# Kernel optimization log

Measured on AMD Instinct MI355X. Metric: run time of the kernel, lower is better.

Reference implementation:

```python
import jax, jax.numpy as jnp
import numpy as np

K = 3      # kernel size (hardcoded 3x3 in the torch module via repeat(...,9,...))
PAD = 1
STRIDE = 1


def _unfold(x):
    # torch.nn.functional.unfold equivalent: (B,C,H,W) -> (B,C,K,K,oh,ow)
    B, C, H, W = x.shape
    p = jax.lax.conv_general_dilated_patches(
        x, (K, K), (STRIDE, STRIDE), ((PAD, PAD), (PAD, PAD)))
    oh, ow = p.shape[2], p.shape[3]
    return p.reshape(B, C, K, K, oh, ow)


def setup_inputs() -> dict:
    key = jax.random.key(0)
    k1, k2, k3, k4 = jax.random.split(key, 4)
    B, Cin, Cout, H, W = 4, 64, 64, 128, 128
    inputs = jax.random.normal(k1, (B, Cin, H, W), jnp.float32)
    depth = jax.random.uniform(k2, (B, 1, H, W), jnp.float32)  # positive depths
    weight = jax.random.uniform(k3, (K, Cout, Cin, K, K), jnp.float32, minval=-0.05, maxval=0.05)
    bias = jax.random.uniform(k4, (Cout,), jnp.float32, minval=-0.05, maxval=0.05)
    return {"inputs": inputs, "depth": depth, "weight": weight, "bias": bias, "f": 1}


def reference(inputs, depth, weight, bias, f):
    # --- DepthKernelFn: per-depth-plane binary masks ---
    depth_wins = _unfold(depth)          # (B,1,K,K,oh,ow)
    s_wins = depth_wins / f              # grid spacing s_i = d / f
    cy, cx = K // 2, K // 2
    d0 = depth_wins[:, :, cy, cx]        # center depth      (B,1,oh,ow)
    s0 = s_wins[:, :, cy, cx]            # center spacing    (B,1,oh,ow)
    offs = jnp.arange(K, dtype=inputs.dtype) - (K - 1) / 2.0  # l - (K-1)/2
    # z_l at center: d0 + (l-1)*s0  -> (K,B,1,oh,ow)
    z0 = d0[None] + offs[:, None, None, None, None] * s0[None]
    half = s0[None] / 2
    a = (z0 - half)[:, :, :, None, None]  # (K,B,1,1,1,oh,ow)
    b = (z0 + half)[:, :, :, None, None]
    dw = depth_wins[None]                 # (1,B,1,K,K,oh,ow)
    # mask_l = 1 where a <= depth < b else 0  (same as the where-cascade in torch)
    mask = ((dw >= a) & (dw < b)).astype(inputs.dtype)  # (K,B,1,K,K,oh,ow)

    # --- RepeatKernelConvFn: masked windowed conv via einsum ---
    inp_wins = _unfold(inputs)            # (B,C,K,K,oh,ow)
    x = inp_wins[None] * mask             # (K,B,C,K,K,oh,ow), depth C=1 broadcasts
    out = jnp.einsum('hijklmn,hojkl->iomn', x, weight)
    out = out + bias.reshape(1, -1, 1, 1)
    return out
```

## Files before the change

kernel.cpp:

```cpp
#include <hip/hip_runtime.h>
#include <math.h>

#define B_N  4
#define CIN  64
#define COUT 64
#define H_N  128
#define W_N  128

typedef _Float16 half8 __attribute__((ext_vector_type(8)));
typedef float    f32x4 __attribute__((ext_vector_type(4)));

#define KTOT   1728
#define NSTEP  54
#define WA_BYTES ((size_t)NSTEP * 4 * 64 * 8 * 2)

__global__ void wprep(const float* __restrict__ w, _Float16* __restrict__ wa) {
    int idx = blockIdx.x * 256 + threadIdx.x;
    if (idx >= NSTEP * 4 * 64) return;
    int lane = idx & 63;
    int mt   = (idx >> 6) & 3;
    int s    = idx >> 8;
    int m    = mt * 16 + (lane & 15);
    int kl0  = (lane >> 4) * 8;
    _Float16 v[8];
#pragma unroll
    for (int j = 0; j < 8; ++j) {
        int k = s * 32 + kl0 + j;
        int g = k >> 6;
        int c = k & 63;
        int t = g / 3;
        int h = g % 3;
        v[j] = (_Float16)w[(((size_t)(h * COUT) + m) * CIN + c) * 9 + t];
    }
    *(int4*)&wa[(size_t)idx * 8] = *(int4*)v;
}

#define XS_LINE 64
#define XS_ROW  (130 * XS_LINE)

__global__ __launch_bounds__(256, 2)
void conv_mfma(const float* __restrict__ inp, const float* __restrict__ depth,
               const _Float16* __restrict__ wa, const float* __restrict__ bias,
               const int* __restrict__ fptr, float* __restrict__ out) {
    __shared__ _Float16 Xs[3 * XS_ROW];

    int bid  = blockIdx.x;
    int y    = bid & (H_N - 1);
    int b    = bid >> 7;
    int tid  = threadIdx.x;
    int lane = tid & 63;
    int wid  = tid >> 6;
    int mh   = wid & 1;
    int nq   = wid >> 1;
    int p0   = nq * 64;
    int ln15 = lane & 15;
    int quad = lane >> 4;

    {
        int x     = tid & 127;
        int chalf = tid >> 7;
        int xi    = x + 1;
        int key   = xi & 7;
        float fbuf[3][32];
#pragma unroll
        for (int dyi = 0; dyi < 3; ++dyi) {
            int yy = y + dyi - 1;
            if (yy >= 0 && yy < H_N) {
                const float* src = inp + (((size_t)b * CIN + chalf * 32) * H_N + yy) * W_N + x;
#pragma unroll
                for (int cc = 0; cc < 32; ++cc)
                    fbuf[dyi][cc] = src[(size_t)cc * H_N * W_N];
            } else {
#pragma unroll
                for (int cc = 0; cc < 32; ++cc) fbuf[dyi][cc] = 0.f;
            }
        }
#pragma unroll
        for (int dyi = 0; dyi < 3; ++dyi) {
            _Float16 hb[32];
#pragma unroll
            for (int cc = 0; cc < 32; ++cc) hb[cc] = (_Float16)fbuf[dyi][cc];
            _Float16* dst = &Xs[dyi * XS_ROW + xi * XS_LINE];
#pragma unroll
            for (int k = 0; k < 4; ++k)
                *(int4*)&dst[((chalf * 4 + k) ^ key) * 8] = *(int4*)&hb[k * 8];
        }
        if (tid < 48) {
            int dyi = tid / 16;
            int rem = tid % 16;
            int xz  = (rem >= 8) ? 129 : 0;
            int k8  = rem & 7;
            int4 z  = {0, 0, 0, 0};
            *(int4*)&Xs[dyi * XS_ROW + xz * XS_LINE + k8 * 8] = z;
        }
    }

    const half8* wa8 = (const half8*)wa;
    half8 A[6][2];
    {
        const half8* bA = wa8 + ((size_t)0 * 24 + mh * 2) * 64 + lane;
#pragma unroll
        for (int j = 0; j < 6; ++j)
#pragma unroll
            for (int mtl = 0; mtl < 2; ++mtl)
                A[j][mtl] = bA[(j * 4 + mtl) * 64];
    }

    double fd = (double)(*fptr);
    unsigned hpk[4];
#pragma unroll
    for (int nt = 0; nt < 4; ++nt) {
        int x = p0 + nt * 16 + ln15;
        float d0f = depth[((size_t)b * H_N + y) * W_N + x];
        double dd  = (double)d0f;
        double inv = fd / dd;
        bool   pos = (inv > 0.0);
        unsigned pk = 0;
        for (int t = 0; t < 9; ++t) {
            int dy = t / 3 - 1, dx = t % 3 - 1;
            int yy = y + dy, xx = x + dx;
            float dwf = (yy >= 0 && yy < H_N && xx >= 0 && xx < W_N)
                        ? depth[((size_t)b * H_N + yy) * W_N + xx] : 0.f;
            int h = -1;
            if (pos) {
                double u  = ((double)dwf - dd) * inv + 1.5;
                double uf = floor(u);
                if (uf >= 0.0 && uf <= 2.0) h = (int)uf;
            }
            pk |= (unsigned)(h + 1) << (2 * t);
        }
        hpk[nt] = pk;
    }

    __syncthreads();

    f32x4 acc[2][4];
#pragma unroll
    for (int mtl = 0; mtl < 2; ++mtl)
#pragma unroll
        for (int nt = 0; nt < 4; ++nt) acc[mtl][nt] = (f32x4){0.f, 0.f, 0.f, 0.f};

    half8 bb[2][8];

#define READ_B(tt) {                                                              \
        int dyi_ = (tt) / 3; int dx_ = (tt) % 3 - 1;                              \
        _Pragma("unroll")                                                         \
        for (int nt_ = 0; nt_ < 4; ++nt_) {                                       \
            int xs_  = p0 + nt_ * 16 + ln15 + dx_ + 1;                            \
            int key_ = xs_ & 7;                                                   \
            int ba_  = dyi_ * XS_ROW + xs_ * XS_LINE;                             \
            bb[(tt) & 1][nt_ * 2 + 0] = *(const half8*)&Xs[ba_ + ((quad    ) ^ key_) * 8]; \
            bb[(tt) & 1][nt_ * 2 + 1] = *(const half8*)&Xs[ba_ + ((quad + 4) ^ key_) * 8]; \
        }                                                                         \
    }

    READ_B(0);

    half8 z8 = {(_Float16)0.f, (_Float16)0.f, (_Float16)0.f, (_Float16)0.f,
                (_Float16)0.f, (_Float16)0.f, (_Float16)0.f, (_Float16)0.f};

#pragma unroll
    for (int t = 0; t < 9; ++t) {
        int hb[4];
#pragma unroll
        for (int nt = 0; nt < 4; ++nt) hb[nt] = (hpk[nt] >> (2 * t)) & 3;

#pragma unroll
        for (int h = 0; h < 3; ++h) {
#pragma unroll
            for (int kk = 0; kk < 2; ++kk) {
                int j = h * 2 + kk;
#pragma unroll
                for (int nt = 0; nt < 4; ++nt) {
                    half8 c = (hb[nt] == h + 1) ? bb[t & 1][nt * 2 + kk] : z8;
                    acc[0][nt] = __builtin_amdgcn_mfma_f32_16x16x32_f16(A[j][0], c, acc[0][nt], 0, 0, 0);
                    acc[1][nt] = __builtin_amdgcn_mfma_f32_16x16x32_f16(A[j][1], c, acc[1][nt], 0, 0, 0);
                }
            }
        }

        if (t < 8) {
            const half8* bA = wa8 + ((size_t)(t + 1) * 24 + mh * 2) * 64 + lane;
#pragma unroll
            for (int j = 0; j < 6; ++j)
#pragma unroll
                for (int mtl = 0; mtl < 2; ++mtl)
                    A[j][mtl] = bA[(j * 4 + mtl) * 64];
            READ_B(t + 1);
            __syncthreads();
        }
    }
#undef READ_B

#pragma unroll
    for (int mtl = 0; mtl < 2; ++mtl) {
#pragma unroll
        for (int nt = 0; nt < 4; ++nt) {
            int x = p0 + nt * 16 + ln15;
#pragma unroll
            for (int r = 0; r < 4; ++r) {
                int o = (mh * 2 + mtl) * 16 + quad * 4 + r;
                out[(((size_t)b * COUT + o) * H_N + y) * W_N + x] = acc[mtl][nt][r] + bias[o];
            }
        }
    }
}

__global__ __launch_bounds__(256)
void conv25d(const float* __restrict__ inp, const float* __restrict__ depth,
             const float* __restrict__ wsrc, const float* __restrict__ bias,
             const int* __restrict__ fptr, float* __restrict__ out) {
    int bid = blockIdx.x;
    int xt  = bid & 3;
    int y   = (bid >> 2) & (H_N - 1);
    int b   = bid >> 9;
    int o   = threadIdx.x & 63;
    int q   = threadIdx.x >> 6;
    int x0  = xt * 32 + q * 8;
    double fd = (double)(*fptr);
    float acc[8];
    float bv = bias[o];
#pragma unroll
    for (int i = 0; i < 8; ++i) acc[i] = bv;
    const float* dcen = depth + ((size_t)b * H_N + y) * W_N;
    float d0[8];
#pragma unroll
    for (int i = 0; i < 8; ++i) d0[i] = dcen[x0 + i];
    for (int t = 0; t < 9; ++t) {
        int dy = t / 3 - 1, dx = t % 3 - 1;
        int yy = y + dy;
        if (yy < 0 || yy >= H_N) continue;
        const float* drow = depth + ((size_t)b * H_N + yy) * W_N;
        int hsel[8];
#pragma unroll
        for (int i = 0; i < 8; ++i) {
            int xx = x0 + i + dx;
            int h = -1;
            if (xx >= 0 && xx < W_N) {
                double dd = (double)d0[i];
                double s0 = dd / fd;
                if (s0 > 0.0) {
                    double u = ((double)drow[xx] - dd) / s0 + 1.5;
                    double uf = floor(u);
                    if (uf >= 0.0 && uf <= 2.0) h = (int)uf;
                }
            }
            hsel[i] = h;
        }
        const float* irow = inp + ((size_t)b * CIN * H_N + yy) * W_N;
        for (int c = 0; c < CIN; ++c) {
            const float* wb = wsrc + ((size_t)o * CIN + c) * 9 + t;
            float w0 = wb[0], w1 = wb[(size_t)COUT * CIN * 9], w2 = wb[2 * (size_t)COUT * CIN * 9];
            const float* ir = irow + (size_t)c * H_N * W_N;
#pragma unroll
            for (int i = 0; i < 8; ++i) {
                int h = hsel[i];
                if (h >= 0) {
                    float wv = (h == 0) ? w0 : ((h == 1) ? w1 : w2);
                    acc[i] = fmaf(ir[x0 + i + dx], wv, acc[i]);
                }
            }
        }
    }
    float* orow = out + (((size_t)b * COUT + o) * H_N + y) * W_N;
#pragma unroll
    for (int i = 0; i < 8; ++i) orow[x0 + i] = acc[i];
}

extern "C" void kernel_launch(void* const* d_in, const int* in_sizes, int n_in,
                              void* d_out, int out_size, void* d_ws, size_t ws_size,
                              hipStream_t stream) {
    const float* inp   = (const float*)d_in[0];
    const float* depth = (const float*)d_in[1];
    const float* w     = (const float*)d_in[2];
    const float* bias  = (const float*)d_in[3];
    const int*   f     = (const int*)d_in[4];
    float* out = (float*)d_out;

    if (ws_size >= WA_BYTES) {
        _Float16* wa = (_Float16*)d_ws;
        wprep<<<NSTEP, 256, 0, stream>>>(w, wa);
        conv_mfma<<<B_N * H_N, 256, 0, stream>>>(inp, depth, wa, bias, f, out);
    } else {
        conv25d<<<B_N * H_N * (W_N / 32), 256, 0, stream>>>(inp, depth, w, bias, f, out);
    }
}
```

Measured before the change: 101.2 us.

## Split MFMA conv blocks into half-row tiles with per-wave output-channel slices

Each block now covers half an output row (64 pixels) instead of a full row, which doubles the grid. Each wave owns one 16-channel output slice across all 64 pixels, so the per-wave accumulator and A-fragment register footprint shrinks. Launch bounds are raised to allow four blocks per CU. The depth-mask computation runs once per pixel in the first wave and is shared through LDS instead of being recomputed redundantly. The loop drops the per-tap __syncthreads and double-buffers the weight fragments. In exchange, the halo columns are reloaded by neighbouring blocks, each block reads the full weight set twice as often overall, and the B reads from LDS are no longer prefetched ahead of the MFMAs.

```diff
diff --git a/kernel.cpp b/kernel.cpp
--- a/kernel.cpp
+++ b/kernel.cpp
@@ -36,82 +36,84 @@
 }
 
 #define XS_LINE 64
-#define XS_ROW  (130 * XS_LINE)
-
-__global__ __launch_bounds__(256, 2)
+#define XS_ROW  (66 * XS_LINE)
+
+__global__ __launch_bounds__(256, 4)
 void conv_mfma(const float* __restrict__ inp, const float* __restrict__ depth,
                const _Float16* __restrict__ wa, const float* __restrict__ bias,
                const int* __restrict__ fptr, float* __restrict__ out) {
     __shared__ _Float16 Xs[3 * XS_ROW];
+    __shared__ unsigned hLds[64];
 
     int bid  = blockIdx.x;
-    int y    = bid & (H_N - 1);
-    int b    = bid >> 7;
+    int xh   = bid & 1;
+    int y    = (bid >> 1) & (H_N - 1);
+    int b    = bid >> 8;
+    int x0   = xh * 64;
     int tid  = threadIdx.x;
     int lane = tid & 63;
-    int wid  = tid >> 6;
-    int mh   = wid & 1;
-    int nq   = wid >> 1;
-    int p0   = nq * 64;
+    int mq   = tid >> 6;
     int ln15 = lane & 15;
     int quad = lane >> 4;
 
     {
-        int x     = tid & 127;
-        int chalf = tid >> 7;
-        int xi    = x + 1;
-        int key   = xi & 7;
-        float fbuf[3][32];
+        int xl  = tid & 63;
+        int cq  = tid >> 6;
+        int xi  = xl + 1;
+        int key = xi & 7;
 #pragma unroll
         for (int dyi = 0; dyi < 3; ++dyi) {
             int yy = y + dyi - 1;
+            _Float16 hb[16];
             if (yy >= 0 && yy < H_N) {
-                const float* src = inp + (((size_t)b * CIN + chalf * 32) * H_N + yy) * W_N + x;
-#pragma unroll
-                for (int cc = 0; cc < 32; ++cc)
-                    fbuf[dyi][cc] = src[(size_t)cc * H_N * W_N];
+                const float* src = inp + (((size_t)b * CIN + cq * 16) * H_N + yy) * W_N + (x0 + xl);
+                float tf[16];
+#pragma unroll
+                for (int cc = 0; cc < 16; ++cc) tf[cc] = src[(size_t)cc * H_N * W_N];
+#pragma unroll
+                for (int cc = 0; cc < 16; ++cc) hb[cc] = (_Float16)tf[cc];
             } else {
 #pragma unroll
-                for (int cc = 0; cc < 32; ++cc) fbuf[dyi][cc] = 0.f;
-            }
-        }
-#pragma unroll
-        for (int dyi = 0; dyi < 3; ++dyi) {
-            _Float16 hb[32];
-#pragma unroll
-            for (int cc = 0; cc < 32; ++cc) hb[cc] = (_Float16)fbuf[dyi][cc];
+                for (int cc = 0; cc < 16; ++cc) hb[cc] = (_Float16)0.f;
+            }
             _Float16* dst = &Xs[dyi * XS_ROW + xi * XS_LINE];
-#pragma unroll
-            for (int k = 0; k < 4; ++k)
-                *(int4*)&dst[((chalf * 4 + k) ^ key) * 8] = *(int4*)&hb[k * 8];
+            *(int4*)&dst[((cq * 2    ) ^ key) * 8] = *(int4*)&hb[0];
+            *(int4*)&dst[((cq * 2 + 1) ^ key) * 8] = *(int4*)&hb[8];
         }
         if (tid < 48) {
-            int dyi = tid / 16;
-            int rem = tid % 16;
-            int xz  = (rem >= 8) ? 129 : 0;
-            int k8  = rem & 7;
-            int4 z  = {0, 0, 0, 0};
-            *(int4*)&Xs[dyi * XS_ROW + xz * XS_LINE + k8 * 8] = z;
+            int dyi  = tid >> 4;
+            int rem  = tid & 15;
+            int side = rem >> 3;
+            int ck   = rem & 7;
+            int xi2  = side ? 65 : 0;
+            int xg   = x0 + xi2 - 1;
+            int key2 = xi2 & 7;
+            int yy   = y + dyi - 1;
+            _Float16 hb[8];
+            if (xg >= 0 && xg < W_N && yy >= 0 && yy < H_N) {
+                const float* src = inp + (((size_t)b * CIN + ck * 8) * H_N + yy) * W_N + xg;
+#pragma unroll
+                for (int cc = 0; cc < 8; ++cc) hb[cc] = (_Float16)src[(size_t)cc * H_N * W_N];
+            } else {
+#pragma unroll
+                for (int cc = 0; cc < 8; ++cc) hb[cc] = (_Float16)0.f;
+            }
+            *(int4*)&Xs[dyi * XS_ROW + xi2 * XS_LINE + (ck ^ key2) * 8] = *(int4*)&hb[0];
         }
     }
 
     const half8* wa8 = (const half8*)wa;
-    half8 A[6][2];
+    half8 Abuf[2][6];
     {
-        const half8* bA = wa8 + ((size_t)0 * 24 + mh * 2) * 64 + lane;
-#pragma unroll
-        for (int j = 0; j < 6; ++j)
-#pragma unroll
-            for (int mtl = 0; mtl < 2; ++mtl)
-                A[j][mtl] = bA[(j * 4 + mtl) * 64];
-    }
-
-    double fd = (double)(*fptr);
-    unsigned hpk[4];
-#pragma unroll
-    for (int nt = 0; nt < 4; ++nt) {
-        int x = p0 + nt * 16 + ln15;
-        float d0f = depth[((size_t)b * H_N + y) * W_N + x];
+        const half8* bA = wa8 + (size_t)mq * 64 + lane;
+#pragma unroll
+        for (int j = 0; j < 6; ++j) Abuf[0][j] = bA[(size_t)j * 4 * 64];
+    }
+
+    if (tid < 64) {
+        int x = x0 + tid;
+        double fd  = (double)(*fptr);
+        float  d0f = depth[((size_t)b * H_N + y) * W_N + x];
         double dd  = (double)d0f;
         double inv = fd / dd;
         bool   pos = (inv > 0.0);
@@ -129,38 +131,43 @@
             }
             pk |= (unsigned)(h + 1) << (2 * t);
         }
-        hpk[nt] = pk;
+        hLds[tid] = pk;
     }
 
     __syncthreads();
 
-    f32x4 acc[2][4];
-#pragma unroll
-    for (int mtl = 0; mtl < 2; ++mtl)
-#pragma unroll
-        for (int nt = 0; nt < 4; ++nt) acc[mtl][nt] = (f32x4){0.f, 0.f, 0.f, 0.f};
-
-    half8 bb[2][8];
-
-#define READ_B(tt) {                                                              \
-        int dyi_ = (tt) / 3; int dx_ = (tt) % 3 - 1;                              \
-        _Pragma("unroll")                                                         \
-        for (int nt_ = 0; nt_ < 4; ++nt_) {                                       \
-            int xs_  = p0 + nt_ * 16 + ln15 + dx_ + 1;                            \
-            int key_ = xs_ & 7;                                                   \
-            int ba_  = dyi_ * XS_ROW + xs_ * XS_LINE;                             \
-            bb[(tt) & 1][nt_ * 2 + 0] = *(const half8*)&Xs[ba_ + ((quad    ) ^ key_) * 8]; \
-            bb[(tt) & 1][nt_ * 2 + 1] = *(const half8*)&Xs[ba_ + ((quad + 4) ^ key_) * 8]; \
-        }                                                                         \
-    }
-
-    READ_B(0);
+    unsigned hpk[4];
+#pragma unroll
+    for (int nt = 0; nt < 4; ++nt) hpk[nt] = hLds[nt * 16 + ln15];
+
+    f32x4 acc[4];
+#pragma unroll
+    for (int nt = 0; nt < 4; ++nt) acc[nt] = (f32x4){0.f, 0.f, 0.f, 0.f};
 
     half8 z8 = {(_Float16)0.f, (_Float16)0.f, (_Float16)0.f, (_Float16)0.f,
                 (_Float16)0.f, (_Float16)0.f, (_Float16)0.f, (_Float16)0.f};
 
 #pragma unroll
     for (int t = 0; t < 9; ++t) {
+        int dyi = t / 3;
+        int dx  = t % 3 - 1;
+
+        half8 bb[8];
+#pragma unroll
+        for (int nt = 0; nt < 4; ++nt) {
+            int xs = nt * 16 + ln15 + dx + 1;
+            int k2 = xs & 7;
+            int ba = dyi * XS_ROW + xs * XS_LINE;
+            bb[nt * 2 + 0] = *(const half8*)&Xs[ba + ((quad    ) ^ k2) * 8];
+            bb[nt * 2 + 1] = *(const half8*)&Xs[ba + ((quad + 4) ^ k2) * 8];
+        }
+
+        if (t < 8) {
+            const half8* bA = wa8 + ((size_t)(t + 1) * 24 + mq) * 64 + lane;
+#pragma unroll
+            for (int j = 0; j < 6; ++j) Abuf[(t + 1) & 1][j] = bA[(size_t)j * 4 * 64];
+        }
+
         int hb[4];
 #pragma unroll
         for (int nt = 0; nt < 4; ++nt) hb[nt] = (hpk[nt] >> (2 * t)) & 3;
@@ -172,36 +179,20 @@
                 int j = h * 2 + kk;
 #pragma unroll
                 for (int nt = 0; nt < 4; ++nt) {
-                    half8 c = (hb[nt] == h + 1) ? bb[t & 1][nt * 2 + kk] : z8;
-                    acc[0][nt] = __builtin_amdgcn_mfma_f32_16x16x32_f16(A[j][0], c, acc[0][nt], 0, 0, 0);
-                    acc[1][nt] = __builtin_amdgcn_mfma_f32_16x16x32_f16(A[j][1], c, acc[1][nt], 0, 0, 0);
+                    half8 c = (hb[nt] == h + 1) ? bb[nt * 2 + kk] : z8;
+                    acc[nt] = __builtin_amdgcn_mfma_f32_16x16x32_f16(Abuf[t & 1][j], c, acc[nt], 0, 0, 0);
                 }
             }
         }
-
-        if (t < 8) {
-            const half8* bA = wa8 + ((size_t)(t + 1) * 24 + mh * 2) * 64 + lane;
-#pragma unroll
-            for (int j = 0; j < 6; ++j)
-#pragma unroll
-                for (int mtl = 0; mtl < 2; ++mtl)
-                    A[j][mtl] = bA[(j * 4 + mtl) * 64];
-            READ_B(t + 1);
-            __syncthreads();
-        }
-    }
-#undef READ_B
-
-#pragma unroll
-    for (int mtl = 0; mtl < 2; ++mtl) {
-#pragma unroll
-        for (int nt = 0; nt < 4; ++nt) {
-            int x = p0 + nt * 16 + ln15;
-#pragma unroll
-            for (int r = 0; r < 4; ++r) {
-                int o = (mh * 2 + mtl) * 16 + quad * 4 + r;
-                out[(((size_t)b * COUT + o) * H_N + y) * W_N + x] = acc[mtl][nt][r] + bias[o];
-            }
+    }
+
+#pragma unroll
+    for (int nt = 0; nt < 4; ++nt) {
+        int x = x0 + nt * 16 + ln15;
+#pragma unroll
+        for (int r = 0; r < 4; ++r) {
+            int o = mq * 16 + quad * 4 + r;
+            out[(((size_t)b * COUT + o) * H_N + y) * W_N + x] = acc[nt][r] + bias[o];
         }
     }
 }
@@ -280,7 +271,7 @@
     if (ws_size >= WA_BYTES) {
         _Float16* wa = (_Float16*)d_ws;
         wprep<<<NSTEP, 256, 0, stream>>>(w, wa);
-        conv_mfma<<<B_N * H_N, 256, 0, stream>>>(inp, depth, wa, bias, f, out);
+        conv_mfma<<<B_N * H_N * 2, 256, 0, stream>>>(inp, depth, wa, bias, f, out);
     } else {
         conv25d<<<B_N * H_N * (W_N / 32), 256, 0, stream>>>(inp, depth, w, bias, f, out);
     }
```

New measurement: 100.2 us. Within noise of the previous version (-1.0%).
